# Performance work log

Measured on AMD Instinct MI355X. Metric: run time of the kernel, lower is better.

The kernel has to match this reference:

```python
import jax, jax.numpy as jnp
import numpy as np
from jax import lax

N, H, W = 16, 112, 112
CIN, COUT, K = 256, 256, 3
STRIDE, PAD = 1, 1


def setup_inputs() -> dict:
    key = jax.random.key(0)
    kx, kw = jax.random.split(key)
    # int8-valued activations and weights, stored as int32 for portable integer conv
    x = jax.random.randint(kx, (N, H, W, CIN), -128, 128, dtype=jnp.int32)
    # weight layout matches the torch module: (out_channels, kH, kW, in_channels) == OHWI
    weight = jax.random.randint(kw, (COUT, K, K, CIN), -128, 128, dtype=jnp.int32)
    return {"x": x, "weight": weight}


def reference(x, weight):
    y = lax.conv_general_dilated(
        x,
        weight,
        window_strides=(STRIDE, STRIDE),
        padding=[(PAD, PAD), (PAD, PAD)],
        dimension_numbers=("NHWC", "OHWI", "NHWC"),
        preferred_element_type=jnp.int32,
    )
    return y  # (N, H, W, COUT) int32
```

## Files before the change

### kernel.cpp

```cpp
#include <hip/hip_runtime.h>
#include <stdint.h>

#define NN   16
#define HH   112
#define WW   112
#define CIN  256
#define COUT 256
#define HP   114
#define WP   114
#define M_TOTAL (NN * HH * WW)
#define XP_BYTES ((size_t)NN * HP * WP * CIN)
#define WPK_BYTES ((size_t)9 * COUT * CIN)

typedef int v4i __attribute__((ext_vector_type(4)));

__device__ __forceinline__ void load_lds16(const void* g, void* l) {
  __builtin_amdgcn_global_load_lds(
      (const __attribute__((address_space(1))) void*)g,
      (__attribute__((address_space(3))) void*)l, 16, 0, 0);
}

__device__ __forceinline__ int pack4(int a, int b, int c, int d) {
  return (a & 255) | ((b & 255) << 8) | ((c & 255) << 16) | (d << 24);
}

__global__ __launch_bounds__(256) void pack_all_kernel(const int* __restrict__ x,
                                                       const int* __restrict__ wgt,
                                                       char* __restrict__ xp,
                                                       char* __restrict__ wp) {
  int bid = blockIdx.x;
  if (bid < 12544) {
    int t = bid * 256 + threadIdx.x;
    int g = t & 15;
    int p = t >> 4;
    int w = p % WW;
    int t2 = p / WW;
    int h = t2 % HH;
    int n = t2 / HH;
    const int4* src = (const int4*)(x + (size_t)t * 16);
    int4 a = src[0], b = src[1], c = src[2], d = src[3];
    int4 ov;
    ov.x = pack4(a.x, a.y, a.z, a.w);
    ov.y = pack4(b.x, b.y, b.z, b.w);
    ov.z = pack4(c.x, c.y, c.z, c.w);
    ov.w = pack4(d.x, d.y, d.z, d.w);
    size_t dst = (((size_t)n * HP + (h + 1)) * WP + (w + 1)) * CIN + (size_t)g * 16;
    *(int4*)(xp + dst) = ov;
  } else if (bid < 12544 + 576) {
    int t = (bid - 12544) * 256 + threadIdx.x;
    int i = t * 4;
    int cout = i / 2304;
    int rem = i - cout * 2304;
    int tap = rem >> 8;
    int ci = rem & 255;
    int4 v = *(const int4*)(wgt + (size_t)i);
    int ov = pack4(v.x, v.y, v.z, v.w);
    int kb = ci >> 6;
    int jg = cout >> 4;
    int l = ((ci >> 4) & 3) * 16 + (cout & 15);
    size_t dst = (((size_t)(tap * 4 + kb) * 16 + jg) * 1024) + (size_t)l * 16 + (ci & 15);
    *(int*)(wp + dst) = ov;
  } else {
    int t = (bid - 13120) * 256 + threadIdx.x;
    int g = t & 15;
    int pix = t >> 4;
    int n = pix / 452;
    int b = pix % 452;
    int h, w;
    if (b < 114) { h = 0; w = b; }
    else if (b < 228) { h = 113; w = b - 114; }
    else { int r = b - 228; h = 1 + (r >> 1); w = (r & 1) ? 113 : 0; }
    size_t dst = (((size_t)n * HP + h) * WP + w) * CIN + (size_t)g * 16;
    *(int4*)(xp + dst) = make_int4(0, 0, 0, 0);
  }
}

__global__ __launch_bounds__(256, 2) void conv_mfma_kernel(const char* __restrict__ xp,
                                                           const char* __restrict__ wp2,
                                                           int* __restrict__ out) {
  __shared__ __align__(16) char As[4 * 8192];
  const int tid = threadIdx.x;
  const int lane = tid & 63;
  const int wave = tid >> 6;
  const int mtile = blockIdx.x;
  const int wm = wave & 1;
  const int wn = wave >> 1;

  const char* gsrcA[2];
#pragma unroll
  for (int q = 0; q < 2; q++) {
    int p = wave * 2048 + q * 1024 + lane * 16;
    int row = p >> 6;
    int colg = ((p >> 4) & 3) ^ ((row >> 1) & 3);
    int m = mtile * 128 + row;
    int w = m % WW;
    int t2 = m / WW;
    int h = t2 % HH;
    int n = t2 / HH;
    gsrcA[q] = xp + (((size_t)n * HP + h) * WP + w) * CIN + (size_t)colg * 16;
  }

  const char* bptr = wp2 + (size_t)(wn * 8) * 1024 + (size_t)lane * 16;

  int aoff[4];
#pragma unroll
  for (int i = 0; i < 4; i++) {
    int r = wm * 64 + i * 16 + (lane & 15);
    aoff[i] = r * 64 + (((lane >> 4) ^ ((r >> 1) & 3)) * 16);
  }

  v4i acc[4][8];
#pragma unroll
  for (int i = 0; i < 4; i++)
#pragma unroll
    for (int j = 0; j < 8; j++) acc[i][j] = (v4i){0, 0, 0, 0};

  auto stageA = [&](int s, int buf) {
    int tap = s >> 2;
    int kb = s & 3;
    int ky = tap / 3;
    int kx = tap - ky * 3;
    int off = (ky * WP + kx) * CIN + kb * 64;
    load_lds16(gsrcA[0] + off, As + buf * 8192 + wave * 2048);
    load_lds16(gsrcA[1] + off, As + buf * 8192 + wave * 2048 + 1024);
  };

  stageA(0, 0);
  stageA(1, 1);
  asm volatile("s_waitcnt vmcnt(2)" ::: "memory");
  __builtin_amdgcn_s_barrier();

#define CONV_STEP(BUF, SB, DOSTAGE, SOA, SBUF, VMN)                                 \
  {                                                                                 \
    const char* Ab = As + (BUF) * 8192;                                             \
    v4i bf[8];                                                                      \
    _Pragma("unroll") for (int j = 0; j < 8; j++)                                   \
        bf[j] = *(const v4i*)(bptr + (size_t)(SB) * 16384 + j * 1024);              \
    v4i af[4];                                                                      \
    _Pragma("unroll") for (int i = 0; i < 4; i++)                                   \
        af[i] = *(const v4i*)(Ab + aoff[i]);                                        \
    __builtin_amdgcn_sched_barrier(0);                                              \
    if (DOSTAGE) {                                                                  \
      load_lds16(gsrcA[0] + (SOA), As + (SBUF) * 8192 + wave * 2048);               \
      load_lds16(gsrcA[1] + (SOA), As + (SBUF) * 8192 + wave * 2048 + 1024);        \
    }                                                                               \
    __builtin_amdgcn_s_setprio(1);                                                  \
    _Pragma("unroll") for (int i = 0; i < 4; i++)                                   \
      _Pragma("unroll") for (int j = 0; j < 8; j++)                                 \
        acc[i][j] = __builtin_amdgcn_mfma_i32_16x16x64_i8(af[i], bf[j],             \
                                                          acc[i][j], 0, 0, 0);      \
    __builtin_amdgcn_s_setprio(0);                                                  \
    asm volatile("s_waitcnt vmcnt(" VMN ")" ::: "memory");                          \
    __builtin_amdgcn_s_barrier();                                                   \
  }

#pragma unroll 1
  for (int g = 0; g < 8; g++) {
    int ky0 = g / 3, kx0 = g - ky0 * 3;
    int oA0 = (ky0 * WP + kx0) * CIN;
    int ky1 = (g + 1) / 3, kx1 = (g + 1) - ky1 * 3;
    int oA1 = (ky1 * WP + kx1) * CIN;
    int sb = 4 * g;
    CONV_STEP(0, sb + 0, true, oA0 + 128, 2, "2")
    CONV_STEP(1, sb + 1, true, oA0 + 192, 3, "2")
    CONV_STEP(2, sb + 2, true, oA1 + 0,   0, "2")
    CONV_STEP(3, sb + 3, true, oA1 + 64,  1, "2")
  }
  {
    int oA8 = (2 * WP + 2) * CIN;
    CONV_STEP(0, 32, true,  oA8 + 128, 2, "2")
    CONV_STEP(1, 33, true,  oA8 + 192, 3, "2")
    CONV_STEP(2, 34, false, 0, 0, "0")
    CONV_STEP(3, 35, false, 0, 0, "0")
  }
#undef CONV_STEP

#pragma unroll
  for (int i = 0; i < 4; i++) {
    const int mg = mtile * 128 + wm * 64 + i * 16 + ((lane >> 4) * 4);
#pragma unroll
    for (int r = 0; r < 4; r++) {
      int* orow = out + (size_t)(mg + r) * COUT + wn * 128 + (lane & 15);
#pragma unroll
      for (int j = 0; j < 8; j++) orow[j * 16] = acc[i][j][r];
    }
  }
}

__global__ void conv_naive_kernel(const int* __restrict__ x, const int* __restrict__ wgt,
                                  int* __restrict__ out, int total) {
  int idx = blockIdx.x * 256 + threadIdx.x;
  if (idx >= total) return;
  int co = idx & 255;
  int p = idx >> 8;
  int w = p % WW;
  int t2 = p / WW;
  int h = t2 % HH;
  int n = t2 / HH;
  int acc = 0;
  for (int ky = 0; ky < 3; ky++) {
    int ih = h + ky - 1;
    if (ih < 0 || ih >= HH) continue;
    for (int kx = 0; kx < 3; kx++) {
      int iw = w + kx - 1;
      if (iw < 0 || iw >= WW) continue;
      const int* xs = x + (((size_t)n * HH + ih) * WW + iw) * CIN;
      const int* ws = wgt + ((size_t)co * 9 + ky * 3 + kx) * CIN;
      for (int ci = 0; ci < CIN; ci++) acc += xs[ci] * ws[ci];
    }
  }
  out[idx] = acc;
}

extern "C" void kernel_launch(void* const* d_in, const int* in_sizes, int n_in,
                              void* d_out, int out_size, void* d_ws, size_t ws_size,
                              hipStream_t stream) {
  const int* x = (const int*)d_in[0];
  const int* wgt = (const int*)d_in[1];
  int* out = (int*)d_out;
  const size_t need = XP_BYTES + WPK_BYTES;
  if (ws_size >= need) {
    char* xp = (char*)d_ws;
    char* wp = xp + XP_BYTES;
    pack_all_kernel<<<13572, 256, 0, stream>>>(x, wgt, xp, wp);
    conv_mfma_kernel<<<M_TOTAL / 128, 256, 0, stream>>>(xp, wp, out);
  } else {
    conv_naive_kernel<<<(out_size + 255) / 256, 256, 0, stream>>>(x, wgt, out, out_size);
  }
}
```

Before: 474.1 us.

## Give each wave private A tiles and prefetch B fragments across steps

Each wave now stages its own 64-row A slice into a private 16KB LDS region, so the per-step block-wide barriers are removed. The low half of the B fragments for the next k-step is prefetched one step ahead into double-buffered registers, so the global load overlaps the MFMAs. In exchange, LDS use doubles to 64KB per block and the A data shared between waves with equal wm is loaded twice. The explicit vmcnt waits before reading LDS are gone, which may leave a race on the staged A data, and occupancy is at risk from the extra LDS and registers.

```diff
diff --git a/kernel.cpp b/kernel.cpp
--- a/kernel.cpp
+++ b/kernel.cpp
@@ -78,21 +78,21 @@
 __global__ __launch_bounds__(256, 2) void conv_mfma_kernel(const char* __restrict__ xp,
                                                            const char* __restrict__ wp2,
                                                            int* __restrict__ out) {
-  __shared__ __align__(16) char As[4 * 8192];
+  __shared__ __align__(16) char As[4 * 16384];
   const int tid = threadIdx.x;
   const int lane = tid & 63;
   const int wave = tid >> 6;
   const int mtile = blockIdx.x;
   const int wm = wave & 1;
   const int wn = wave >> 1;
-
-  const char* gsrcA[2];
-#pragma unroll
-  for (int q = 0; q < 2; q++) {
-    int p = wave * 2048 + q * 1024 + lane * 16;
-    int row = p >> 6;
-    int colg = ((p >> 4) & 3) ^ ((row >> 1) & 3);
-    int m = mtile * 128 + row;
+  char* const myAs = As + wave * 16384;
+
+  const char* gsrcA[4];
+#pragma unroll
+  for (int q = 0; q < 4; q++) {
+    int rl = q * 16 + (lane >> 2);
+    int colg = (lane & 3) ^ ((rl >> 1) & 3);
+    int m = mtile * 128 + wm * 64 + rl;
     int w = m % WW;
     int t2 = m / WW;
     int h = t2 % HH;
@@ -105,7 +105,7 @@
   int aoff[4];
 #pragma unroll
   for (int i = 0; i < 4; i++) {
-    int r = wm * 64 + i * 16 + (lane & 15);
+    int r = i * 16 + (lane & 15);
     aoff[i] = r * 64 + (((lane >> 4) ^ ((r >> 1) & 3)) * 16);
   }
 
@@ -115,43 +115,44 @@
 #pragma unroll
     for (int j = 0; j < 8; j++) acc[i][j] = (v4i){0, 0, 0, 0};
 
-  auto stageA = [&](int s, int buf) {
-    int tap = s >> 2;
-    int kb = s & 3;
-    int ky = tap / 3;
-    int kx = tap - ky * 3;
-    int off = (ky * WP + kx) * CIN + kb * 64;
-    load_lds16(gsrcA[0] + off, As + buf * 8192 + wave * 2048);
-    load_lds16(gsrcA[1] + off, As + buf * 8192 + wave * 2048 + 1024);
-  };
-
-  stageA(0, 0);
-  stageA(1, 1);
-  asm volatile("s_waitcnt vmcnt(2)" ::: "memory");
-  __builtin_amdgcn_s_barrier();
-
-#define CONV_STEP(BUF, SB, DOSTAGE, SOA, SBUF, VMN)                                 \
-  {                                                                                 \
-    const char* Ab = As + (BUF) * 8192;                                             \
-    v4i bf[8];                                                                      \
-    _Pragma("unroll") for (int j = 0; j < 8; j++)                                   \
-        bf[j] = *(const v4i*)(bptr + (size_t)(SB) * 16384 + j * 1024);              \
-    v4i af[4];                                                                      \
-    _Pragma("unroll") for (int i = 0; i < 4; i++)                                   \
-        af[i] = *(const v4i*)(Ab + aoff[i]);                                        \
-    __builtin_amdgcn_sched_barrier(0);                                              \
-    if (DOSTAGE) {                                                                  \
-      load_lds16(gsrcA[0] + (SOA), As + (SBUF) * 8192 + wave * 2048);               \
-      load_lds16(gsrcA[1] + (SOA), As + (SBUF) * 8192 + wave * 2048 + 1024);        \
-    }                                                                               \
-    __builtin_amdgcn_s_setprio(1);                                                  \
-    _Pragma("unroll") for (int i = 0; i < 4; i++)                                   \
-      _Pragma("unroll") for (int j = 0; j < 8; j++)                                 \
-        acc[i][j] = __builtin_amdgcn_mfma_i32_16x16x64_i8(af[i], bf[j],             \
-                                                          acc[i][j], 0, 0, 0);      \
-    __builtin_amdgcn_s_setprio(0);                                                  \
-    asm volatile("s_waitcnt vmcnt(" VMN ")" ::: "memory");                          \
-    __builtin_amdgcn_s_barrier();                                                   \
+  v4i bfX[4], bfY[4];
+
+#define STAGE_A(AOFF, B)                                                     \
+  { _Pragma("unroll") for (int q = 0; q < 4; q++)                            \
+      load_lds16(gsrcA[q] + (AOFF), myAs + (B) * 4096 + q * 1024); }
+
+  STAGE_A(0, 0)
+#pragma unroll
+  for (int j = 0; j < 4; j++) bfX[j] = *(const v4i*)(bptr + j * 1024);
+  STAGE_A(64, 1)
+  asm volatile("s_waitcnt vmcnt(8)" ::: "memory");
+  __builtin_amdgcn_sched_barrier(0);
+
+#define CONV_STEP(BUF, SB, LO_CUR, LO_NXT, DO_LON, DO_AST, AOFF2, ABUF2)     \
+  {                                                                          \
+    const char* Ab = myAs + (BUF) * 4096;                                    \
+    v4i af[4];                                                               \
+    _Pragma("unroll") for (int i = 0; i < 4; i++)                            \
+        af[i] = *(const v4i*)(Ab + aoff[i]);                                 \
+    v4i bhi[4];                                                              \
+    _Pragma("unroll") for (int j = 0; j < 4; j++)                            \
+        bhi[j] = *(const v4i*)(bptr + (size_t)(SB) * 16384 + (4 + j) * 1024);\
+    if (DO_LON) {                                                            \
+      _Pragma("unroll") for (int j = 0; j < 4; j++)                          \
+          LO_NXT[j] = *(const v4i*)(bptr + (size_t)((SB) + 1) * 16384 + j * 1024); \
+    }                                                                        \
+    if (DO_AST) STAGE_A(AOFF2, ABUF2)                                        \
+    __builtin_amdgcn_s_setprio(1);                                           \
+    _Pragma("unroll") for (int i = 0; i < 4; i++)                            \
+      _Pragma("unroll") for (int j = 0; j < 4; j++)                          \
+        acc[i][j] = __builtin_amdgcn_mfma_i32_16x16x64_i8(af[i], LO_CUR[j],  \
+                                                          acc[i][j], 0, 0, 0); \
+    _Pragma("unroll") for (int i = 0; i < 4; i++)                            \
+      _Pragma("unroll") for (int j = 0; j < 4; j++)                          \
+        acc[i][4 + j] = __builtin_amdgcn_mfma_i32_16x16x64_i8(af[i], bhi[j], \
+                                                              acc[i][4 + j], 0, 0, 0); \
+    __builtin_amdgcn_s_setprio(0);                                           \
+    __builtin_amdgcn_sched_barrier(0);                                       \
   }
 
 #pragma unroll 1
@@ -161,19 +162,20 @@
     int ky1 = (g + 1) / 3, kx1 = (g + 1) - ky1 * 3;
     int oA1 = (ky1 * WP + kx1) * CIN;
     int sb = 4 * g;
-    CONV_STEP(0, sb + 0, true, oA0 + 128, 2, "2")
-    CONV_STEP(1, sb + 1, true, oA0 + 192, 3, "2")
-    CONV_STEP(2, sb + 2, true, oA1 + 0,   0, "2")
-    CONV_STEP(3, sb + 3, true, oA1 + 64,  1, "2")
+    CONV_STEP(0, sb + 0, bfX, bfY, true, true, oA0 + 128, 2)
+    CONV_STEP(1, sb + 1, bfY, bfX, true, true, oA0 + 192, 3)
+    CONV_STEP(2, sb + 2, bfX, bfY, true, true, oA1 + 0,   0)
+    CONV_STEP(3, sb + 3, bfY, bfX, true, true, oA1 + 64,  1)
   }
   {
     int oA8 = (2 * WP + 2) * CIN;
-    CONV_STEP(0, 32, true,  oA8 + 128, 2, "2")
-    CONV_STEP(1, 33, true,  oA8 + 192, 3, "2")
-    CONV_STEP(2, 34, false, 0, 0, "0")
-    CONV_STEP(3, 35, false, 0, 0, "0")
+    CONV_STEP(0, 32, bfX, bfY, true,  true,  oA8 + 128, 2)
+    CONV_STEP(1, 33, bfY, bfX, true,  true,  oA8 + 192, 3)
+    CONV_STEP(2, 34, bfX, bfY, true,  false, 0, 0)
+    CONV_STEP(3, 35, bfY, bfX, false, false, 0, 0)
   }
 #undef CONV_STEP
+#undef STAGE_A
 
 #pragma unroll
   for (int i = 0; i < 4; i++) {
```

New measurement: 459.2 us. 1.03x faster.
